# Performance work log

Measured on AMD Instinct MI355X. Metric: run time of the kernel, lower is better.

Reference implementation:

```python
import jax, jax.numpy as jnp
import numpy as np

H, W_RFFT = 14, 8  # spatial grid 14x14, rfft2 last-dim width = 14//2+1


def setup_inputs() -> dict:
    key = jax.random.key(0)
    k1, k2 = jax.random.split(key)
    B, N, C = 256, 196, 512
    x = jax.random.normal(k1, (B, N, C), dtype=jnp.float32)
    complex_weight = jax.random.normal(k2, (H, W_RFFT, C, 2), dtype=jnp.float32) * 0.02
    return {"x": x, "complex_weight": complex_weight}


def reference(x, complex_weight):
    B, N, C = x.shape
    a = b = int(np.sqrt(N))  # 14
    xg = x.reshape(B, a, b, C).astype(jnp.float32)
    # rfft2 over spatial dims with ortho normalization
    xf = jnp.fft.rfft2(xg, axes=(1, 2), norm="ortho")  # [B, a, b//2+1, C] complex
    weight = complex_weight[..., 0] + 1j * complex_weight[..., 1]  # [a, b//2+1, C]
    xf = xf * weight
    xo = jnp.fft.irfft2(xf, s=(a, b), axes=(1, 2), norm="ortho")  # [B, a, b, C] real
    return xo.astype(x.dtype).reshape(B, N, C)
```

## Files before the change

### kernel.cpp

```cpp
#include <hip/hip_runtime.h>
#include <hip/hip_bf16.h>


#define Hs 14
#define Ns 196
#define Cc 512
#define CT 32
#define CONV_THREADS 448

typedef float v2f __attribute__((ext_vector_type(2)));

__global__ __launch_bounds__(256) void prep_a_kernel(const float* __restrict__ cw,
                                                     float* __restrict__ T) {
    __shared__ float cs[14], sn[14];
    if (threadIdx.x < 14) {
        float ang = (float)threadIdx.x * 0.44879895051282760549f;
        cs[threadIdx.x] = cosf(ang);
        sn[threadIdx.x] = sinf(ang);
    }
    __syncthreads();

    int gid = blockIdx.x * 256 + threadIdx.x;
    int c = gid & 511;
    int s = gid >> 9;
    int h = s / 14;
    int dn = s % 14;
    int h2 = (h == 0) ? 0 : (14 - h);

    float Tr = 0.0f, Ti = 0.0f;
    int k = 0;
    #pragma unroll
    for (int w = 0; w < 8; ++w) {
        const float* p = cw + (size_t)(((h * 8 + w) * 512 + c) * 2);
        float Wr = p[0], Wi = p[1];
        Tr += Wr * cs[k] - Wi * sn[k];
        Ti += Wr * sn[k] + Wi * cs[k];
        k += dn; if (k >= 14) k -= 14;
    }
    int k2 = dn; if (k2 >= 14) k2 -= 14;
    #pragma unroll
    for (int w = 1; w < 7; ++w) {
        const float* p = cw + (size_t)(((h2 * 8 + w) * 512 + c) * 2);
        float Wr = p[0], Wi = p[1];
        Tr += Wr * cs[k2] - Wi * sn[k2];
        Ti -= Wr * sn[k2] + Wi * cs[k2];
        k2 += dn; if (k2 >= 14) k2 -= 14;
    }
    float* o = T + (size_t)(s * 512 + c) * 2;
    o[0] = Tr;
    o[1] = Ti;
}

__global__ __launch_bounds__(256) void prep_b_kernel(const float* __restrict__ T,
                                                     float* __restrict__ R) {
    __shared__ float cs[14], sn[14];
    if (threadIdx.x < 14) {
        float ang = (float)threadIdx.x * 0.44879895051282760549f;
        cs[threadIdx.x] = cosf(ang);
        sn[threadIdx.x] = sinf(ang);
    }
    __syncthreads();

    int gid = blockIdx.x * 256 + threadIdx.x;
    int c = gid & 511;
    int s = gid >> 9;
    int dm = s / 14;
    int dn = s % 14;

    float acc = 0.0f;
    int kh = 0;
    #pragma unroll
    for (int h = 0; h < 14; ++h) {
        const float* p = T + (size_t)(((h * 14 + dn) * 512 + c) * 2);
        acc += p[0] * cs[kh] - p[1] * sn[kh];
        kh += dm; if (kh >= 14) kh -= 14;
    }
    R[s * 512 + c] = acc * (1.0f / 196.0f);
}

__global__ __launch_bounds__(CONV_THREADS, 3) void conv_kernel(
        const float* __restrict__ x,
        const float* __restrict__ R,
        float* __restrict__ out) {
    __shared__ float xs[2 * Ns * CT];
    __shared__ float rs[Ns * CT];

    const int bx = blockIdx.x;
    const int ct = bx & 15;
    const int bp = bx >> 4;
    const int c0 = ct * CT;
    const int b0 = bp * 2;
    const int t  = threadIdx.x;

    const float* xb = x + (size_t)b0 * Ns * Cc + c0;
    const float* Rb = R + c0;
    for (int i = t; i < Ns * CT; i += CONV_THREADS) {
        int pq = i >> 5;
        int cc = i & (CT - 1);
        xs[i]           = xb[pq * Cc + cc];
        xs[Ns * CT + i] = xb[Ns * Cc + pq * Cc + cc];
        rs[i]           = Rb[pq * Cc + cc];
    }
    __syncthreads();

    const int c = t & (CT - 1);
    const int r = t >> 5;
    const int bsel = (r >= 7) ? 1 : 0;
    const int m = r - 7 * bsel;
    const float* xsb = xs + bsel * Ns * CT;

    v2f acc[14];
    #pragma unroll
    for (int n = 0; n < 14; ++n) acc[n] = 0.0f;

    #pragma unroll 1
    for (int p = 0; p < 14; ++p) {
        int dm1 = m - p; if (dm1 < 0) dm1 += 14;
        int dm2 = dm1 + 7; if (dm2 >= 14) dm2 -= 14;
        v2f Rr[14];
        #pragma unroll
        for (int dn = 0; dn < 14; ++dn) {
            Rr[dn].x = rs[(dm1 * 14 + dn) * CT + c];
            Rr[dn].y = rs[(dm2 * 14 + dn) * CT + c];
        }
        #pragma unroll
        for (int q = 0; q < 14; ++q) {
            float xv = xsb[(p * 14 + q) * CT + c];
            v2f xv2 = {xv, xv};
            #pragma unroll
            for (int n = 0; n < 14; ++n) {
                acc[n] += xv2 * Rr[(n - q + 14) % 14];
            }
        }
    }

    const int b = b0 + bsel;
    float* o1 = out + ((size_t)b * Ns + m * 14) * Cc + c0 + c;
    float* o2 = o1 + (size_t)(7 * 14) * Cc;
    #pragma unroll
    for (int n = 0; n < 14; ++n) {
        o1[n * Cc] = acc[n].x;
        o2[n * Cc] = acc[n].y;
    }
}

extern "C" void kernel_launch(void* const* d_in, const int* in_sizes, int n_in,
                              void* d_out, int out_size, void* d_ws, size_t ws_size,
                              hipStream_t stream) {
    const float* x  = (const float*)d_in[0];
    const float* cw = (const float*)d_in[1];
    float* outp = (float*)d_out;
    float* R = (float*)d_ws;
    float* T = R + (size_t)Ns * Cc;

    prep_a_kernel<<<392, 256, 0, stream>>>(cw, T);
    prep_b_kernel<<<392, 256, 0, stream>>>(T, R);
    conv_kernel<<<128 * 16, CONV_THREADS, 0, stream>>>(x, R, outp);
}
```

Baseline: 269.8 us.

## Pack both batch samples into v2f in shared memory for conv register blocking

Interleaves the two batch elements' x values as float2 in LDS, so each thread computes one output row m for both batches at once instead of two rows (m, m+7) of a single batch. The R value becomes the broadcast operand and the packed x pair supplies the two lanes of the packed FMA. Each p iteration now loads 14 float2 x values and 14 R floats. Before, it loaded 28 R values and 14 x floats, which cuts scalar LDS reads, but the 8-byte LDS accesses may change the bank-conflict pattern.

```diff
diff --git a/kernel.cpp b/kernel.cpp
--- a/kernel.cpp
+++ b/kernel.cpp
@@ -82,7 +82,7 @@
         const float* __restrict__ x,
         const float* __restrict__ R,
         float* __restrict__ out) {
-    __shared__ float xs[2 * Ns * CT];
+    __shared__ v2f  xs2[Ns * CT];
     __shared__ float rs[Ns * CT];
 
     const int bx = blockIdx.x;
@@ -97,17 +97,16 @@
     for (int i = t; i < Ns * CT; i += CONV_THREADS) {
         int pq = i >> 5;
         int cc = i & (CT - 1);
-        xs[i]           = xb[pq * Cc + cc];
-        xs[Ns * CT + i] = xb[Ns * Cc + pq * Cc + cc];
-        rs[i]           = Rb[pq * Cc + cc];
+        v2f v;
+        v.x = xb[pq * Cc + cc];
+        v.y = xb[(size_t)Ns * Cc + pq * Cc + cc];
+        xs2[i] = v;
+        rs[i]  = Rb[pq * Cc + cc];
     }
     __syncthreads();
 
     const int c = t & (CT - 1);
-    const int r = t >> 5;
-    const int bsel = (r >= 7) ? 1 : 0;
-    const int m = r - 7 * bsel;
-    const float* xsb = xs + bsel * Ns * CT;
+    const int m = t >> 5;
 
     v2f acc[14];
     #pragma unroll
@@ -115,32 +114,34 @@
 
     #pragma unroll 1
     for (int p = 0; p < 14; ++p) {
-        int dm1 = m - p; if (dm1 < 0) dm1 += 14;
-        int dm2 = dm1 + 7; if (dm2 >= 14) dm2 -= 14;
-        v2f Rr[14];
+        int dm = m - p; if (dm < 0) dm += 14;
+        const v2f*  xrow = xs2 + p  * 14 * CT + c;
+        const float* rrow = rs  + dm * 14 * CT + c;
+
+        v2f xr[14];
+        #pragma unroll
+        for (int q = 0; q < 14; ++q) xr[q] = xrow[q * CT];
+
+        float rv[14];
+        #pragma unroll
+        for (int dn = 0; dn < 14; ++dn) rv[dn] = rrow[dn * CT];
+
         #pragma unroll
         for (int dn = 0; dn < 14; ++dn) {
-            Rr[dn].x = rs[(dm1 * 14 + dn) * CT + c];
-            Rr[dn].y = rs[(dm2 * 14 + dn) * CT + c];
-        }
-        #pragma unroll
-        for (int q = 0; q < 14; ++q) {
-            float xv = xsb[(p * 14 + q) * CT + c];
-            v2f xv2 = {xv, xv};
+            v2f R2 = {rv[dn], rv[dn]};
             #pragma unroll
             for (int n = 0; n < 14; ++n) {
-                acc[n] += xv2 * Rr[(n - q + 14) % 14];
+                acc[n] += xr[(n - dn + 14) % 14] * R2;
             }
         }
     }
 
-    const int b = b0 + bsel;
-    float* o1 = out + ((size_t)b * Ns + m * 14) * Cc + c0 + c;
-    float* o2 = o1 + (size_t)(7 * 14) * Cc;
+    float* o0 = out + ((size_t)b0 * Ns + m * 14) * Cc + c0 + c;
+    float* o1 = o0 + (size_t)Ns * Cc;
     #pragma unroll
     for (int n = 0; n < 14; ++n) {
-        o1[n * Cc] = acc[n].x;
-        o2[n * Cc] = acc[n].y;
+        o0[n * Cc] = acc[n].x;
+        o1[n * Cc] = acc[n].y;
     }
 }
 
```

Result: no change. 273.1 us (+1.2%).
